# Kernel optimization log

Hardware: AMD Instinct MI355X
Metric: run time of the kernel (lower is better)

The kernel has to match this reference:

```python
import jax, jax.numpy as jnp
import numpy as np

B, H, IN, T_MAX = 256, 768, 192, 128


def setup_inputs() -> dict:
    key = jax.random.key(0)
    ks = jax.random.split(key, 9)
    s = 1.0 / np.sqrt(H)  # torch GRUCell/Linear uniform(-1/sqrt(H),1/sqrt(H)) scale
    context = jax.random.normal(ks[0], (B, H), dtype=jnp.float32)
    weight_ih = jax.random.normal(ks[1], (3 * H, IN), dtype=jnp.float32) * s
    weight_hh = jax.random.normal(ks[2], (3 * H, H), dtype=jnp.float32) * s
    bias_ih = jax.random.normal(ks[3], (3 * H,), dtype=jnp.float32) * s
    bias_hh = jax.random.normal(ks[4], (3 * H,), dtype=jnp.float32) * s
    fc_w = jax.random.normal(ks[5], (1, H), dtype=jnp.float32) * s
    fc_b = jax.random.normal(ks[6], (1,), dtype=jnp.float32) * s
    num_pred_list = jax.random.randint(ks[7], (B,), 1, T_MAX + 1).astype(jnp.int32)
    num_pred_list = num_pred_list.at[0].set(T_MAX)  # pin max so pad width == T_MAX+2
    return {
        "context": context,
        "weight_ih": weight_ih,
        "weight_hh": weight_hh,
        "bias_ih": bias_ih,
        "bias_hh": bias_hh,
        "fc_w": fc_w,
        "fc_b": fc_b,
        "num_pred_list": num_pred_list,
        "max_steps": T_MAX,
    }


def _deltas(context, weight_hh, bias_ih, bias_hh, fc_w, fc_b, T):
    # GRU input is the frozen zero vector, so x-gates reduce to bias_ih.
    Bh, H_ = context.shape
    gi_r, gi_z, gi_n = bias_ih[:H_], bias_ih[H_:2 * H_], bias_ih[2 * H_:]
    Whh_T = weight_hh.T  # [H, 3H]

    def step(h, _):
        gh = h @ Whh_T + bias_hh  # [B, 3H]
        r = jax.nn.sigmoid(gi_r + gh[:, :H_])
        z = jax.nn.sigmoid(gi_z + gh[:, H_:2 * H_])
        n = jnp.tanh(gi_n + r * gh[:, 2 * H_:])
        h_new = (1.0 - z) * n + z * h
        delta = jax.nn.softplus(h_new @ fc_w[0] + fc_b[0])  # [B]
        return h_new, delta

    _, deltas = jax.lax.scan(step, context, None, length=T)
    return deltas.T  # [B, T]


def reference(context, weight_ih, weight_hh, bias_ih, bias_hh, fc_w, fc_b, num_pred_list, max_steps):
    T = int(max_steps)
    Bh = context.shape[0]
    deltas = _deltas(context, weight_hh, bias_ih, bias_hh, fc_w, fc_b, T)  # [B,T]
    cum = jnp.cumsum(deltas, axis=1)
    n = num_pred_list  # [B]
    last = jnp.take_along_axis(cum, jnp.clip(n - 1, 0, T - 1)[:, None], axis=1)  # [B,1]
    norm = cum / (last + 1e-6)
    valid = jnp.arange(T)[None, :] < n[:, None]
    body = jnp.where(valid, norm, 0.0)  # [B,T]
    out = jnp.zeros((Bh, T + 2), dtype=context.dtype)
    out = out.at[:, 1:T + 1].set(body)
    out = out.at[jnp.arange(Bh), n + 1].set(1.0)  # trailing 1.0 per sequence
    return out
```

## Files before the change

kernel.cpp:

```cpp
#include <hip/hip_runtime.h>
#include <stdint.h>

#define Bn 256
#define Hn 768
#define Tn 128
#define KS 24
#define CBn 48
#define RGn 4
#define ROWS 64
#define NTHR 256
#define SMEM_BYTES 147456
#define SUBW 64

typedef __attribute__((ext_vector_type(8))) short short8;
typedef __attribute__((ext_vector_type(4))) float floatx4;

static __device__ __forceinline__ unsigned short f2bf(float f) {
  unsigned int x = __float_as_uint(f);
  x += 0x7fffu + ((x >> 16) & 1u);
  return (unsigned short)(x >> 16);
}
static __device__ __forceinline__ float bf2f(unsigned short u) {
  return __uint_as_float(((unsigned int)u) << 16);
}

__global__ void swz_w(const float* __restrict__ W,
                      unsigned short* __restrict__ whi,
                      unsigned short* __restrict__ wlo) {
  int i = blockIdx.x * blockDim.x + threadIdx.x;
  if (i >= 2304 * (Hn / 8)) return;
  int n  = i / (Hn / 8);
  int k0 = (i % (Hn / 8)) * 8;
  int tile = n >> 4, kstep = k0 >> 5;
  int lane = (n & 15) + (((k0 >> 3) & 3) << 4);
  size_t off = ((size_t)(tile * KS + kstep)) * 512 + (size_t)lane * 8;
  const float* src = W + (size_t)n * Hn + k0;
  short8 h8, l8;
#pragma unroll
  for (int q = 0; q < 8; ++q) {
    float w = src[q];
    unsigned short hb = f2bf(w);
    h8[q] = (short)hb;
    l8[q] = (short)f2bf(w - bf2f(hb));
  }
  *(short8*)(whi + off) = h8;
  *(short8*)(wlo + off) = l8;
}

__global__ void init_h(const float* __restrict__ ctx,
                       unsigned short* __restrict__ hhi,
                       unsigned short* __restrict__ hlo,
                       float* __restrict__ ddot, unsigned* __restrict__ cnt) {
  int i = blockIdx.x * blockDim.x + threadIdx.x;
  if (i < Bn * Hn) {
    float c = ctx[i];
    unsigned short hb = f2bf(c);
    hhi[i] = hb;
    hlo[i] = f2bf(c - bf2f(hb));
  }
  if (i < Tn * Bn) ddot[i] = 0.f;
  if (i < RGn * 8 * SUBW) cnt[i] = 0u;
}

__global__ __launch_bounds__(NTHR, 1) void gru_persist(
    const unsigned short* __restrict__ whi, const unsigned short* __restrict__ wlo,
    unsigned short* hhi0, unsigned short* hlo0,
    unsigned short* hhi1, unsigned short* hlo1,
    const float* __restrict__ bias_ih, const float* __restrict__ bias_hh,
    const float* __restrict__ fc_w, float* __restrict__ ddot,
    unsigned* __restrict__ cnt) {
  extern __shared__ char smem[];
  unsigned short* lds_w = (unsigned short*)smem;

  const int cb = blockIdx.x;
  const int rg = blockIdx.y;
  const int tid = threadIdx.x;
  const int lane = tid & 63;
  const int wave = tid >> 6;
  const int ln15 = lane & 15, quad = lane >> 4;
  const int row0 = rg * ROWS;
  const int j0 = cb * 16;

  for (int u = tid; u < 144 * 64; u += NTHR) {
    int c = u >> 6, w = u & 63;
    int plane = c & 1;
    int ks = (c >> 1) % KS;
    int g  = c / (2 * KS);
    const unsigned short* src =
        (plane ? wlo : whi) + ((size_t)((g * CBn + cb) * KS + ks)) * 512 + (size_t)w * 8;
    *(short8*)(lds_w + (size_t)c * 512 + w * 8) = *(const short8*)src;
  }

  const int j = j0 + ln15;
  const float bir = bias_ih[j], biz = bias_ih[Hn + j], bin = bias_ih[2 * Hn + j];
  const float bhr = bias_hh[j], bhz = bias_hh[Hn + j], bhn = bias_hh[2 * Hn + j];
  const float fw = fc_w[j];
  const int mrow0 = row0 + wave * 16;

  unsigned short* HHI[2] = {hhi0, hhi1};
  unsigned short* HLO[2] = {hlo0, hlo1};
  unsigned* mycnt = cnt + rg * 8 * SUBW;

  __syncthreads();

  int p = 0;
  for (int t = 0; t < Tn; ++t) {
    const unsigned short* Ah_base = HHI[p] + (size_t)(mrow0 + ln15) * Hn + quad * 8;
    const unsigned short* Al_base = HLO[p] + (size_t)(mrow0 + ln15) * Hn + quad * 8;

    unsigned short hoh[4], hol[4];
#pragma unroll
    for (int i = 0; i < 4; ++i) {
      size_t idx = (size_t)(mrow0 + quad * 4 + i) * Hn + j;
      hoh[i] = HHI[p][idx];
      hol[i] = HLO[p][idx];
    }

    floatx4 acc[3];
#pragma unroll
    for (int g = 0; g < 3; ++g) acc[g] = (floatx4){0.f, 0.f, 0.f, 0.f};

    short8 Abh[2][4], Abl[2][4];
#pragma unroll
    for (int q = 0; q < 4; ++q) {
      Abh[0][q] = *(const short8*)(Ah_base + q * 32);
      Abl[0][q] = *(const short8*)(Al_base + q * 32);
    }
#pragma unroll
    for (int c = 0; c < 6; ++c) {
      const int cur = c & 1, nxt = cur ^ 1;
      if (c < 5) {
#pragma unroll
        for (int q = 0; q < 4; ++q) {
          Abh[nxt][q] = *(const short8*)(Ah_base + ((c + 1) * 4 + q) * 32);
          Abl[nxt][q] = *(const short8*)(Al_base + ((c + 1) * 4 + q) * 32);
        }
      }
#pragma unroll
      for (int kk = 0; kk < 4; ++kk) {
        const int ks = c * 4 + kk;
#pragma unroll
        for (int g = 0; g < 3; ++g) {
          const int cbase = ((g * KS + ks) * 2) * 512 + lane * 8;
          short8 Bh = *(const short8*)(lds_w + cbase);
          short8 Bl = *(const short8*)(lds_w + cbase + 512);
          acc[g] = __builtin_amdgcn_mfma_f32_16x16x32_bf16(Abh[cur][kk], Bh, acc[g], 0, 0, 0);
          acc[g] = __builtin_amdgcn_mfma_f32_16x16x32_bf16(Abl[cur][kk], Bh, acc[g], 0, 0, 0);
          acc[g] = __builtin_amdgcn_mfma_f32_16x16x32_bf16(Abh[cur][kk], Bl, acc[g], 0, 0, 0);
        }
      }
    }

    float fcv[4];
#pragma unroll
    for (int i = 0; i < 4; ++i) {
      const int r = mrow0 + quad * 4 + i;
      float gr = bir + bhr + acc[0][i];
      float gz = biz + bhz + acc[1][i];
      float rr = 1.f / (1.f + __expf(-gr));
      float zz = 1.f / (1.f + __expf(-gz));
      float gn = bin + rr * (acc[2][i] + bhn);
      float nn = 1.f - 2.f / (1.f + __expf(2.f * gn));
      float hold = bf2f(hoh[i]) + bf2f(hol[i]);
      float hn = (1.f - zz) * nn + zz * hold;
      size_t idx = (size_t)r * Hn + j;
      unsigned short hb = f2bf(hn);
      HHI[p ^ 1][idx] = hb;
      HLO[p ^ 1][idx] = f2bf(hn - bf2f(hb));
      fcv[i] = hn * fw;
    }
#pragma unroll
    for (int i = 0; i < 4; ++i) {
      fcv[i] += __shfl_xor(fcv[i], 1);
      fcv[i] += __shfl_xor(fcv[i], 2);
      fcv[i] += __shfl_xor(fcv[i], 4);
      fcv[i] += __shfl_xor(fcv[i], 8);
    }
    if (ln15 == 0) {
#pragma unroll
      for (int i = 0; i < 4; ++i)
        atomicAdd(&ddot[t * Bn + mrow0 + quad * 4 + i], fcv[i]);
    }

    __syncthreads();
    if (tid == 0)
      __hip_atomic_fetch_add(&mycnt[(cb >> 3) * SUBW], 1u, __ATOMIC_RELEASE,
                             __HIP_MEMORY_SCOPE_AGENT);
    if (wave == 0) {
      const unsigned tgt = 8u * (unsigned)(t + 1);
      while (true) {
        unsigned v = (lane < 6)
            ? __hip_atomic_load(&mycnt[lane * SUBW], __ATOMIC_RELAXED,
                                __HIP_MEMORY_SCOPE_AGENT)
            : tgt;
        if (__ballot(v >= tgt) == ~0ull) break;
        __builtin_amdgcn_s_sleep(1);
      }
    }
    if (tid == 0)
      (void)__hip_atomic_load(&mycnt[0], __ATOMIC_ACQUIRE, __HIP_MEMORY_SCOPE_AGENT);
    __syncthreads();
    p ^= 1;
  }
}

__global__ void post_k(const float* __restrict__ ddot,
                       const float* __restrict__ fc_b,
                       const int* __restrict__ npred, float* __restrict__ out) {
  const int b = blockIdx.x;
  const int t = threadIdx.x;
  __shared__ float s[Tn];
  float x = ddot[(size_t)t * Bn + b] + fc_b[0];
  float sp = (x > 20.f) ? x : log1pf(__expf(x));
  s[t] = sp;
  __syncthreads();
  for (int off = 1; off < Tn; off <<= 1) {
    float v = s[t];
    float add = (t >= off) ? s[t - off] : 0.f;
    __syncthreads();
    s[t] = v + add;
    __syncthreads();
  }
  const int n = npred[b];
  const float last = s[n - 1] + 1e-6f;
  float body = (t < n) ? (s[t] / last) : 0.f;
  float* ob = out + (size_t)b * (Tn + 2);
  ob[1 + t] = body;
  if (t == 0) { ob[0] = 0.f; ob[Tn + 1] = 0.f; }
  __syncthreads();
  if (t == 0) ob[n + 1] = 1.f;
}

extern "C" void kernel_launch(void* const* d_in, const int* in_sizes, int n_in,
                              void* d_out, int out_size, void* d_ws, size_t ws_size,
                              hipStream_t stream) {
  const float* context   = (const float*)d_in[0];
  const float* weight_hh = (const float*)d_in[2];
  const float* bias_ih   = (const float*)d_in[3];
  const float* bias_hh   = (const float*)d_in[4];
  const float* fc_w      = (const float*)d_in[5];
  const float* fc_b      = (const float*)d_in[6];
  const int*   npred     = (const int*)d_in[7];
  float* out = (float*)d_out;

  char* ws = (char*)d_ws;
  size_t o = 0;
  unsigned short* hhi0 = (unsigned short*)(ws + o); o += (size_t)Bn * Hn * 2;
  unsigned short* hlo0 = (unsigned short*)(ws + o); o += (size_t)Bn * Hn * 2;
  unsigned short* hhi1 = (unsigned short*)(ws + o); o += (size_t)Bn * Hn * 2;
  unsigned short* hlo1 = (unsigned short*)(ws + o); o += (size_t)Bn * Hn * 2;
  unsigned short* whi  = (unsigned short*)(ws + o); o += (size_t)3 * Hn * Hn * 2;
  unsigned short* wlo  = (unsigned short*)(ws + o); o += (size_t)3 * Hn * Hn * 2;
  float* ddot = (float*)(ws + o); o += (size_t)Tn * Bn * 4;
  unsigned* cntp = (unsigned*)(ws + o); o += (size_t)RGn * 8 * SUBW * 4;

  swz_w<<<dim3((2304 * (Hn / 8) + 255) / 256), dim3(256), 0, stream>>>(weight_hh, whi, wlo);
  init_h<<<dim3((Bn * Hn + 255) / 256), dim3(256), 0, stream>>>(context, hhi0, hlo0, ddot, cntp);

  hipFuncSetAttribute((const void*)gru_persist,
                      hipFuncAttributeMaxDynamicSharedMemorySize, SMEM_BYTES);
  void* kargs[] = {(void*)&whi, (void*)&wlo, (void*)&hhi0, (void*)&hlo0,
                   (void*)&hhi1, (void*)&hlo1, (void*)&bias_ih, (void*)&bias_hh,
                   (void*)&fc_w, (void*)&ddot, (void*)&cntp};
  hipLaunchCooperativeKernel((const void*)gru_persist, dim3(CBn, RGn), dim3(NTHR),
                             kargs, SMEM_BYTES, stream);

  post_k<<<dim3(Bn), dim3(Tn), 0, stream>>>(ddot, fc_b, npred, out);
}
```

Before: 2.410 ms.

## Merge row groups into one 1024-thread block per column slice, keep h in registers

The persistent GRU kernel no longer splits the batch across four row-group blocks. It launches 48 blocks of 1024 threads, and each block covers all 256 batch rows for its 16-column slice. Each weight slice is then loaded into LDS once per column block instead of four times. The fp32 previous hidden value for each owned element is kept in registers across steps rather than reloaded from the bf16 hi/lo buffers, which removes per-step global loads and the round-off from the split representation. The cost is that only 48 CUs take part, each doing four times the MFMA work per step, and the launch-bounds change may constrain register allocation.

Result: slower. 3.993 ms (+65.7%).

```diff
diff --git a/kernel.cpp b/kernel.cpp
--- a/kernel.cpp
+++ b/kernel.cpp
@@ -6,9 +6,7 @@
 #define Tn 128
 #define KS 24
 #define CBn 48
-#define RGn 4
-#define ROWS 64
-#define NTHR 256
+#define NTHR 1024
 #define SMEM_BYTES 147456
 #define SUBW 64
 
@@ -48,37 +46,33 @@
 }
 
 __global__ void init_h(const float* __restrict__ ctx,
-                       unsigned short* __restrict__ hhi,
-                       unsigned short* __restrict__ hlo,
+                       unsigned short* __restrict__ hbase,
                        float* __restrict__ ddot, unsigned* __restrict__ cnt) {
   int i = blockIdx.x * blockDim.x + threadIdx.x;
   if (i < Bn * Hn) {
     float c = ctx[i];
     unsigned short hb = f2bf(c);
-    hhi[i] = hb;
-    hlo[i] = f2bf(c - bf2f(hb));
+    hbase[i] = hb;
+    hbase[Bn * Hn + i] = f2bf(c - bf2f(hb));
   }
   if (i < Tn * Bn) ddot[i] = 0.f;
-  if (i < RGn * 8 * SUBW) cnt[i] = 0u;
-}
-
-__global__ __launch_bounds__(NTHR, 1) void gru_persist(
+  if (i < 8 * SUBW) cnt[i] = 0u;
+}
+
+__global__ __launch_bounds__(NTHR, 4) void gru_persist(
     const unsigned short* __restrict__ whi, const unsigned short* __restrict__ wlo,
-    unsigned short* hhi0, unsigned short* hlo0,
-    unsigned short* hhi1, unsigned short* hlo1,
+    unsigned short* hbase,
     const float* __restrict__ bias_ih, const float* __restrict__ bias_hh,
-    const float* __restrict__ fc_w, float* __restrict__ ddot,
-    unsigned* __restrict__ cnt) {
+    const float* __restrict__ fc_w, const float* __restrict__ ctx,
+    float* __restrict__ ddot, unsigned* __restrict__ cnt) {
   extern __shared__ char smem[];
   unsigned short* lds_w = (unsigned short*)smem;
 
   const int cb = blockIdx.x;
-  const int rg = blockIdx.y;
   const int tid = threadIdx.x;
   const int lane = tid & 63;
   const int wave = tid >> 6;
   const int ln15 = lane & 15, quad = lane >> 4;
-  const int row0 = rg * ROWS;
   const int j0 = cb * 16;
 
   for (int u = tid; u < 144 * 64; u += NTHR) {
@@ -95,11 +89,16 @@
   const float bir = bias_ih[j], biz = bias_ih[Hn + j], bin = bias_ih[2 * Hn + j];
   const float bhr = bias_hh[j], bhz = bias_hh[Hn + j], bhn = bias_hh[2 * Hn + j];
   const float fw = fc_w[j];
-  const int mrow0 = row0 + wave * 16;
-
-  unsigned short* HHI[2] = {hhi0, hhi1};
-  unsigned short* HLO[2] = {hlo0, hlo1};
-  unsigned* mycnt = cnt + rg * 8 * SUBW;
+  const int mrow0 = wave * 16;
+
+  float hold[4];
+#pragma unroll
+  for (int i = 0; i < 4; ++i)
+    hold[i] = ctx[(size_t)(mrow0 + quad * 4 + i) * Hn + j];
+
+  const size_t N = (size_t)Bn * Hn;
+  unsigned short* HHI[2] = {hbase, hbase + 2 * N};
+  unsigned short* HLO[2] = {hbase + N, hbase + 3 * N};
 
   __syncthreads();
 
@@ -107,14 +106,6 @@
   for (int t = 0; t < Tn; ++t) {
     const unsigned short* Ah_base = HHI[p] + (size_t)(mrow0 + ln15) * Hn + quad * 8;
     const unsigned short* Al_base = HLO[p] + (size_t)(mrow0 + ln15) * Hn + quad * 8;
-
-    unsigned short hoh[4], hol[4];
-#pragma unroll
-    for (int i = 0; i < 4; ++i) {
-      size_t idx = (size_t)(mrow0 + quad * 4 + i) * Hn + j;
-      hoh[i] = HHI[p][idx];
-      hol[i] = HLO[p][idx];
-    }
 
     floatx4 acc[3];
 #pragma unroll
@@ -161,8 +152,8 @@
       float zz = 1.f / (1.f + __expf(-gz));
       float gn = bin + rr * (acc[2][i] + bhn);
       float nn = 1.f - 2.f / (1.f + __expf(2.f * gn));
-      float hold = bf2f(hoh[i]) + bf2f(hol[i]);
-      float hn = (1.f - zz) * nn + zz * hold;
+      float hn = (1.f - zz) * nn + zz * hold[i];
+      hold[i] = hn;
       size_t idx = (size_t)r * Hn + j;
       unsigned short hb = f2bf(hn);
       HHI[p ^ 1][idx] = hb;
@@ -184,13 +175,13 @@
 
     __syncthreads();
     if (tid == 0)
-      __hip_atomic_fetch_add(&mycnt[(cb >> 3) * SUBW], 1u, __ATOMIC_RELEASE,
+      __hip_atomic_fetch_add(&cnt[(cb >> 3) * SUBW], 1u, __ATOMIC_RELEASE,
                              __HIP_MEMORY_SCOPE_AGENT);
     if (wave == 0) {
       const unsigned tgt = 8u * (unsigned)(t + 1);
       while (true) {
         unsigned v = (lane < 6)
-            ? __hip_atomic_load(&mycnt[lane * SUBW], __ATOMIC_RELAXED,
+            ? __hip_atomic_load(&cnt[lane * SUBW], __ATOMIC_RELAXED,
                                 __HIP_MEMORY_SCOPE_AGENT)
             : tgt;
         if (__ballot(v >= tgt) == ~0ull) break;
@@ -198,7 +189,7 @@
       }
     }
     if (tid == 0)
-      (void)__hip_atomic_load(&mycnt[0], __ATOMIC_ACQUIRE, __HIP_MEMORY_SCOPE_AGENT);
+      (void)__hip_atomic_load(&cnt[0], __ATOMIC_ACQUIRE, __HIP_MEMORY_SCOPE_AGENT);
     __syncthreads();
     p ^= 1;
   }
@@ -245,24 +236,21 @@
 
   char* ws = (char*)d_ws;
   size_t o = 0;
-  unsigned short* hhi0 = (unsigned short*)(ws + o); o += (size_t)Bn * Hn * 2;
-  unsigned short* hlo0 = (unsigned short*)(ws + o); o += (size_t)Bn * Hn * 2;
-  unsigned short* hhi1 = (unsigned short*)(ws + o); o += (size_t)Bn * Hn * 2;
-  unsigned short* hlo1 = (unsigned short*)(ws + o); o += (size_t)Bn * Hn * 2;
-  unsigned short* whi  = (unsigned short*)(ws + o); o += (size_t)3 * Hn * Hn * 2;
-  unsigned short* wlo  = (unsigned short*)(ws + o); o += (size_t)3 * Hn * Hn * 2;
+  unsigned short* hbase = (unsigned short*)(ws + o); o += (size_t)4 * Bn * Hn * 2;
+  unsigned short* whi   = (unsigned short*)(ws + o); o += (size_t)3 * Hn * Hn * 2;
+  unsigned short* wlo   = (unsigned short*)(ws + o); o += (size_t)3 * Hn * Hn * 2;
   float* ddot = (float*)(ws + o); o += (size_t)Tn * Bn * 4;
-  unsigned* cntp = (unsigned*)(ws + o); o += (size_t)RGn * 8 * SUBW * 4;
+  unsigned* cntp = (unsigned*)(ws + o); o += (size_t)8 * SUBW * 4;
 
   swz_w<<<dim3((2304 * (Hn / 8) + 255) / 256), dim3(256), 0, stream>>>(weight_hh, whi, wlo);
-  init_h<<<dim3((Bn * Hn + 255) / 256), dim3(256), 0, stream>>>(context, hhi0, hlo0, ddot, cntp);
+  init_h<<<dim3((Bn * Hn + 255) / 256), dim3(256), 0, stream>>>(context, hbase, ddot, cntp);
 
   hipFuncSetAttribute((const void*)gru_persist,
                       hipFuncAttributeMaxDynamicSharedMemorySize, SMEM_BYTES);
-  void* kargs[] = {(void*)&whi, (void*)&wlo, (void*)&hhi0, (void*)&hlo0,
-                   (void*)&hhi1, (void*)&hlo1, (void*)&bias_ih, (void*)&bias_hh,
-                   (void*)&fc_w, (void*)&ddot, (void*)&cntp};
-  hipLaunchCooperativeKernel((const void*)gru_persist, dim3(CBn, RGn), dim3(NTHR),
+  void* kargs[] = {(void*)&whi, (void*)&wlo, (void*)&hbase, (void*)&bias_ih,
+                   (void*)&bias_hh, (void*)&fc_w, (void*)&context, (void*)&ddot,
+                   (void*)&cntp};
+  hipLaunchCooperativeKernel((const void*)gru_persist, dim3(CBn), dim3(NTHR),
                              kargs, SMEM_BYTES, stream);
 
   post_k<<<dim3(Bn), dim3(Tn), 0, stream>>>(ddot, fc_b, npred, out);
```
